# Optimization experiments

Measured on AMD Instinct MI355X. Metric: run time of the kernel, lower is better.

The kernel has to match this reference:

```python
import jax, jax.numpy as jnp
import numpy as np

N_SLOTS = 64
DECAY = 0.999
B, S, H, M = 4, 4096, 2048, 128


def _l2norm(t, eps=1e-12):
    return t / jnp.maximum(jnp.linalg.norm(t, axis=-1, keepdims=True), eps)


def setup_inputs() -> dict:
    key = jax.random.key(0)
    ks = jax.random.split(key, 6)
    return {
        "x": jax.random.normal(ks[0], (B, S, H), dtype=jnp.float32),
        "W_query": jax.random.normal(ks[1], (M, H), dtype=jnp.float32) * 0.02,
        "W_key": jax.random.normal(ks[2], (M, H), dtype=jnp.float32) * 0.02,
        "W_value": jax.random.normal(ks[3], (M, H), dtype=jnp.float32) * 0.02,
        "W_out": jax.random.normal(ks[4], (H, M), dtype=jnp.float32) * 0.02,
        "W_gate_w": jax.random.normal(ks[5], (1, H), dtype=jnp.float32) * 0.02,
        "W_gate_b": jnp.full((1,), -2.0, dtype=jnp.float32),
        "log_beta": jnp.full((1,), np.log(8.0), dtype=jnp.float32),
        "chunk_size": 64,
    }


def reference(x, W_query, W_key, W_value, W_out, W_gate_w, W_gate_b, log_beta, chunk_size):
    b, s, h = x.shape
    m = W_query.shape[0]
    dt = x.dtype

    q = x @ W_query.T                      # (b, s, m)
    k = _l2norm(x @ W_key.T)               # (b, s, m)
    v = _l2norm(x @ W_value.T)             # (b, s, m)
    gate = jax.nn.sigmoid(x @ W_gate_w.T + W_gate_b)  # (b, s, 1)
    beta = jnp.exp(log_beta).reshape(())

    nc = s // chunk_size
    decay_c = jnp.asarray(DECAY, dt) ** chunk_size

    def chunkify(t):
        # (b, s, d) -> (nc, b, chunk, d)
        return jnp.moveaxis(t.reshape(b, nc, chunk_size, -1), 1, 0)

    qc, kc, vc = chunkify(q), chunkify(k), chunkify(v)
    wc = chunkify(gate)[..., 0]            # (nc, b, chunk)

    K0 = jnp.zeros((N_SLOTS, m), dt)
    V0 = jnp.zeros((N_SLOTS, m), dt)
    s0 = jnp.zeros((N_SLOTS,), dt)
    ptr0 = jnp.asarray(0, jnp.int32)

    def step(carry, inp):
        K_mem, V_mem, mem_strength, ptr = carry
        qch, kch, vch, wch = inp           # (b,c,m) x3, (b,c)
        # --- read: softmax retrieval over active slots ---
        slot_mask = (mem_strength > 1e-8).astype(dt)           # (n_slots,)
        scores = jnp.einsum("bcm,nm->bcn", qch, K_mem) * beta
        scores = scores + (1.0 - slot_mask) * -1e9
        attn = jax.nn.softmax(scores, axis=-1)
        r = jnp.einsum("bcn,nm->bcm", attn, V_mem)
        r = jnp.where(mem_strength.sum() < 1e-8, jnp.zeros_like(r), r)
        # --- write: gated aggregation into one slot ---
        w_sum = jnp.maximum(wch.sum(), 1e-8)
        k_agg = _l2norm((kch * wch[..., None]).sum((0, 1)) / w_sum)
        v_agg = _l2norm((vch * wch[..., None]).sum((0, 1)) / w_sum)
        write_str = wch.mean()
        mem_strength = mem_strength * decay_c
        slot = ptr % N_SLOTS
        K_mem = K_mem.at[slot].set(k_agg)
        V_mem = V_mem.at[slot].set(v_agg)
        mem_strength = mem_strength.at[slot].set(write_str)
        return (K_mem, V_mem, mem_strength, ptr + 1), (r, write_str)

    _, (rs, wss) = jax.lax.scan(step, (K0, V0, s0, ptr0), (qc, kc, vc, wc))

    retrieved = jnp.moveaxis(rs, 0, 1).reshape(b, s, m)
    out = retrieved @ W_out.T              # (b, s, h)
    # clamp output norm to 10
    onorm = jnp.maximum(jnp.linalg.norm(out, axis=-1, keepdims=True), 1e-6)
    out = out * jnp.minimum(10.0 / onorm, 1.0)
    mean_ws = jnp.mean(wss)
    return out, mean_ws
```

## Files before the change

### kernel.cpp

```cpp
#include <hip/hip_runtime.h>
#include <math.h>
#include <stdint.h>

#define NTOK 16384
#define SEQ  4096
#define HD   2048
#define MD   128
#define NCH  64
#define CHK  64

typedef __attribute__((ext_vector_type(8))) _Float16 half8;
typedef __attribute__((ext_vector_type(4))) float floatx4;

__device__ __forceinline__ void gload_lds16(const void* g, void* l) {
    __builtin_amdgcn_global_load_lds(
        (const __attribute__((address_space(1))) unsigned int*)(uintptr_t)g,
        (__attribute__((address_space(3))) unsigned int*)(uintptr_t)l,
        16, 0, 0);
}

__global__ __launch_bounds__(256) void convert_w_kernel(
    const float* __restrict__ Wq, const float* __restrict__ Wk,
    const float* __restrict__ Wv, const float* __restrict__ Wo,
    _Float16* __restrict__ Wcath, _Float16* __restrict__ Woh)
{
    int i = blockIdx.x * 256 + threadIdx.x;
    if (i < 384 * HD) {
        int r = i >> 11;
        float val;
        if (r < 128)      val = Wq[i];
        else if (r < 256) val = Wk[i - 128 * HD];
        else              val = Wv[i - 256 * HD];
        Wcath[i] = (_Float16)val;
    } else {
        int j = i - 384 * HD;
        Woh[j] = (_Float16)Wo[j];
    }
}

__global__ __launch_bounds__(128) void gmat_kernel(
    const float* __restrict__ Wo, float* __restrict__ G)
{
    __shared__ float col[HD];
    int a = blockIdx.x;
    int b = threadIdx.x;
    for (int j = b; j < HD; j += 128) col[j] = Wo[(size_t)j * MD + a];
    __syncthreads();
    float s = 0.f;
    for (int j = 0; j < HD; ++j) s = fmaf(col[j], Wo[(size_t)j * MD + b], s);
    G[a * MD + b] = s;
}

__global__ __launch_bounds__(256, 1) void gemm_proj_mfma(
    const float* __restrict__ x, const _Float16* __restrict__ Wcath,
    const float* __restrict__ Wgw, const float* __restrict__ gb,
    float* __restrict__ q, float* __restrict__ k, float* __restrict__ v,
    float* __restrict__ wg)
{
    __shared__ _Float16 As[2][64 * 64];
    __shared__ _Float16 Bs[2][3][128 * 64];
    floatx4 acc[3][2][4];
    #pragma unroll
    for (int p = 0; p < 3; ++p)
        #pragma unroll
        for (int i = 0; i < 2; ++i)
            #pragma unroll
            for (int j = 0; j < 4; ++j) acc[p][i][j] = (floatx4){0.f, 0.f, 0.f, 0.f};

    const int tid  = threadIdx.x;
    const int wave = tid >> 6, lane = tid & 63;
    const int wm = wave & 1, wn = wave >> 1;
    const int row0 = blockIdx.x * 64;

    const int ar0 = tid >> 3;
    const int ac0 = (tid & 7) ^ (ar0 & 7);
    const float* xA0 = x + (size_t)(row0 + ar0) * HD + ac0 * 8;
    const float* xA1 = x + (size_t)(row0 + ar0 + 32) * HD + ac0 * 8;
    const float* wgp = Wgw + ac0 * 8;

    float gacc0 = 0.f, gacc1 = 0.f;
    float4 a00, a01, a10, a11, g0, g1;

#define STAGE_B(buf_, k0_) do {                                               \
        _Pragma("unroll")                                                     \
        for (int p = 0; p < 3; ++p) {                                         \
            _Pragma("unroll")                                                 \
            for (int rnd = 0; rnd < 4; ++rnd) {                               \
                int sg = rnd * 4 + wave;                                      \
                int br = sg * 8 + (lane >> 3);                                \
                int bc = (lane & 7) ^ (br & 7);                               \
                gload_lds16(Wcath + (size_t)(p * 128 + br) * HD + (k0_) + bc * 8, \
                            (char*)Bs[buf_][p] + sg * 1024);                  \
            }                                                                 \
        } } while (0)

#define LOAD_A(k0_) do {                                                      \
        a00 = *(const float4*)(xA0 + (k0_));                                  \
        a01 = *(const float4*)(xA0 + (k0_) + 4);                              \
        a10 = *(const float4*)(xA1 + (k0_));                                  \
        a11 = *(const float4*)(xA1 + (k0_) + 4);                              \
        g0 = *(const float4*)(wgp + (k0_));                                   \
        g1 = *(const float4*)(wgp + (k0_) + 4);                               \
    } while (0)

#define FINISH_A(buf_) do {                                                   \
        gacc0 += a00.x*g0.x + a00.y*g0.y + a00.z*g0.z + a00.w*g0.w            \
               + a01.x*g1.x + a01.y*g1.y + a01.z*g1.z + a01.w*g1.w;           \
        gacc1 += a10.x*g0.x + a10.y*g0.y + a10.z*g0.z + a10.w*g0.w            \
               + a11.x*g1.x + a11.y*g1.y + a11.z*g1.z + a11.w*g1.w;           \
        half8 h0, h1;                                                         \
        h0[0] = (_Float16)a00.x; h0[1] = (_Float16)a00.y;                     \
        h0[2] = (_Float16)a00.z; h0[3] = (_Float16)a00.w;                     \
        h0[4] = (_Float16)a01.x; h0[5] = (_Float16)a01.y;                     \
        h0[6] = (_Float16)a01.z; h0[7] = (_Float16)a01.w;                     \
        h1[0] = (_Float16)a10.x; h1[1] = (_Float16)a10.y;                     \
        h1[2] = (_Float16)a10.z; h1[3] = (_Float16)a10.w;                     \
        h1[4] = (_Float16)a11.x; h1[5] = (_Float16)a11.y;                     \
        h1[6] = (_Float16)a11.z; h1[7] = (_Float16)a11.w;                     \
        *(half8*)((char*)As[buf_] + tid * 16)        = h0;                    \
        *(half8*)((char*)As[buf_] + 4096 + tid * 16) = h1;                    \
    } while (0)

#define COMPUTE(buf_) do {                                                    \
        half8 af[2][2];                                                       \
        _Pragma("unroll")                                                     \
        for (int i = 0; i < 2; ++i) {                                         \
            int r  = wm * 32 + i * 16 + (lane & 15);                          \
            int rb = r * 128 + (lane >> 4) * 16;                              \
            int sw = (r & 7) << 4;                                            \
            af[i][0] = *(const half8*)((const char*)As[buf_] + ( rb       ^ sw)); \
            af[i][1] = *(const half8*)((const char*)As[buf_] + ((rb + 64) ^ sw)); \
        }                                                                     \
        _Pragma("unroll")                                                     \
        for (int p = 0; p < 3; ++p) {                                         \
            half8 bf[4][2];                                                   \
            _Pragma("unroll")                                                 \
            for (int j = 0; j < 4; ++j) {                                     \
                int r  = wn * 64 + j * 16 + (lane & 15);                      \
                int rb = r * 128 + (lane >> 4) * 16;                          \
                int sw = (r & 7) << 4;                                        \
                bf[j][0] = *(const half8*)((const char*)Bs[buf_][p] + ( rb       ^ sw)); \
                bf[j][1] = *(const half8*)((const char*)Bs[buf_][p] + ((rb + 64) ^ sw)); \
            }                                                                 \
            _Pragma("unroll")                                                 \
            for (int ks = 0; ks < 2; ++ks)                                    \
                _Pragma("unroll")                                             \
                for (int i = 0; i < 2; ++i)                                   \
                    _Pragma("unroll")                                         \
                    for (int j = 0; j < 4; ++j)                               \
                        acc[p][i][j] = __builtin_amdgcn_mfma_f32_16x16x32_f16(\
                            af[i][ks], bf[j][ks], acc[p][i][j], 0, 0, 0);     \
        }                                                                     \
    } while (0)

    STAGE_B(0, 0);
    LOAD_A(0);
    FINISH_A(0);
    __syncthreads();

    int cur = 0;
    for (int t = 0; t < HD / 64; ++t) {
        if (t < HD / 64 - 1) {
            STAGE_B(cur ^ 1, (t + 1) * 64);
            LOAD_A((t + 1) * 64);
        }
        COMPUTE(cur);
        if (t < HD / 64 - 1) FINISH_A(cur ^ 1);
        __syncthreads();
        cur ^= 1;
    }

    gacc0 += __shfl_xor(gacc0, 1);
    gacc0 += __shfl_xor(gacc0, 2);
    gacc0 += __shfl_xor(gacc0, 4);
    gacc1 += __shfl_xor(gacc1, 1);
    gacc1 += __shfl_xor(gacc1, 2);
    gacc1 += __shfl_xor(gacc1, 4);
    if ((tid & 7) == 0) {
        wg[row0 + ar0]      = 1.f / (1.f + expf(-(gacc0 + gb[0])));
        wg[row0 + ar0 + 32] = 1.f / (1.f + expf(-(gacc1 + gb[0])));
    }

    #pragma unroll
    for (int p = 0; p < 3; ++p) {
        float* dst = (p == 0) ? q : ((p == 1) ? k : v);
        #pragma unroll
        for (int i = 0; i < 2; ++i) {
            int m = row0 + wm * 32 + i * 16 + (lane >> 4) * 4;
            #pragma unroll
            for (int j = 0; j < 4; ++j) {
                int c = wn * 64 + j * 16 + (lane & 15);
                #pragma unroll
                for (int r = 0; r < 4; ++r)
                    dst[(size_t)(m + r) * MD + c] = acc[p][i][j][r];
            }
        }
    }
#undef STAGE_B
#undef LOAD_A
#undef FINISH_A
#undef COMPUTE
}

__global__ __launch_bounds__(256) void normsig_kernel(
    float* __restrict__ k, float* __restrict__ v)
{
    int wave = threadIdx.x >> 6, lane = threadIdx.x & 63;
    int row = blockIdx.x * 4 + wave;
    size_t base = (size_t)row * MD + lane * 2;
    float2 k2 = *reinterpret_cast<float2*>(&k[base]);
    float2 v2 = *reinterpret_cast<float2*>(&v[base]);
    float ks = k2.x * k2.x + k2.y * k2.y;
    float vs = v2.x * v2.x + v2.y * v2.y;
    #pragma unroll
    for (int off = 32; off > 0; off >>= 1) {
        ks += __shfl_xor(ks, off);
        vs += __shfl_xor(vs, off);
    }
    float ki = 1.f / fmaxf(sqrtf(ks), 1e-12f);
    float vi = 1.f / fmaxf(sqrtf(vs), 1e-12f);
    k2.x *= ki; k2.y *= ki; v2.x *= vi; v2.y *= vi;
    *reinterpret_cast<float2*>(&k[base]) = k2;
    *reinterpret_cast<float2*>(&v[base]) = v2;
}

__global__ __launch_bounds__(256) void agg_part_kernel(
    const float* __restrict__ kn, const float* __restrict__ vn,
    const float* __restrict__ w,
    float* __restrict__ kpart, float* __restrict__ vpart,
    float* __restrict__ wpart)
{
    int t = blockIdx.x >> 2, b = blockIdx.x & 3;
    int tid = threadIdx.x;
    int d = tid & 127, h = tid >> 7;
    int base_row = b * SEQ + t * CHK;

    float ka = 0.f, va = 0.f;
    for (int c = h * 32; c < h * 32 + 32; ++c) {
        int row = base_row + c;
        float wv = w[row];
        ka = fmaf(wv, kn[(size_t)row * MD + d], ka);
        va = fmaf(wv, vn[(size_t)row * MD + d], va);
    }
    __shared__ float sk[128], sv[128];
    if (h == 1) { sk[d] = ka; sv[d] = va; }
    __syncthreads();
    if (h == 0) {
        kpart[(size_t)blockIdx.x * 128 + d] = ka + sk[d];
        vpart[(size_t)blockIdx.x * 128 + d] = va + sv[d];
    }
    if (tid < 64) {
        float wv = w[base_row + tid];
        #pragma unroll
        for (int off = 32; off > 0; off >>= 1) wv += __shfl_xor(wv, off);
        if (tid == 0) wpart[blockIdx.x] = wv;
    }
}

__global__ __launch_bounds__(128) void agg_combine_kernel(
    const float* __restrict__ kpart, const float* __restrict__ vpart,
    const float* __restrict__ wpart,
    float* __restrict__ kaT, float* __restrict__ vagg, float* __restrict__ wstr)
{
    int t = blockIdx.x;
    int d = threadIdx.x;
    int wave = d >> 6, lane = d & 63;
    float ku = 0.f, vu = 0.f;
    #pragma unroll
    for (int b = 0; b < 4; ++b) {
        ku += kpart[(size_t)(t * 4 + b) * 128 + d];
        vu += vpart[(size_t)(t * 4 + b) * 128 + d];
    }
    float wsum = wpart[t * 4] + wpart[t * 4 + 1] + wpart[t * 4 + 2] + wpart[t * 4 + 3];
    float winv = 1.f / fmaxf(wsum, 1e-8f);
    ku *= winv; vu *= winv;

    __shared__ float red[4];
    float ks = ku * ku, vs = vu * vu;
    #pragma unroll
    for (int off = 32; off > 0; off >>= 1) {
        ks += __shfl_xor(ks, off);
        vs += __shfl_xor(vs, off);
    }
    if (lane == 0) { red[wave] = ks; red[2 + wave] = vs; }
    __syncthreads();
    float kinv = 1.f / fmaxf(sqrtf(red[0] + red[1]), 1e-12f);
    float vinv = 1.f / fmaxf(sqrtf(red[2] + red[3]), 1e-12f);
    kaT[d * NCH + t] = ku * kinv;
    vagg[t * MD + d] = vu * vinv;
    if (d == 0) wstr[t] = wsum * (1.f / 256.f);
}

__global__ __launch_bounds__(64) void meanws_kernel(
    const float* __restrict__ wstr, float* __restrict__ outp)
{
    int lane = threadIdx.x;
    float v = wstr[lane];
    #pragma unroll
    for (int off = 32; off > 0; off >>= 1) v += __shfl_xor(v, off);
    if (lane == 0) outp[0] = v * (1.f / 64.f);
}

__global__ __launch_bounds__(512, 1) void attn_kernel(
    const float* __restrict__ q, const float* __restrict__ kaT,
    const float* __restrict__ vagg, const float* __restrict__ G,
    const float* __restrict__ logbeta, _Float16* __restrict__ rsh16)
{
    __shared__ float kaT_s[MD * NCH];
    __shared__ float vagg_s[NCH * MD];
    __shared__ float G_s[MD * MD];
    __shared__ float qs[8][MD];
    __shared__ float attn_sh[8][64];
    __shared__ float rsh_sh[8][MD];

    const int tid  = threadIdx.x;
    const int wave = tid >> 6, lane = tid & 63;
    const int row0 = blockIdx.x * 64;
    const int t = (row0 & (SEQ - 1)) >> 6;
    const float beta = expf(logbeta[0]);

    {
        const float4* s0 = (const float4*)kaT;
        const float4* s1 = (const float4*)vagg;
        const float4* s2 = (const float4*)G;
        float4* d0 = (float4*)kaT_s;
        float4* d1 = (float4*)vagg_s;
        float4* d2 = (float4*)G_s;
        #pragma unroll
        for (int i = 0; i < 4; ++i) {
            d0[tid + i * 512] = s0[tid + i * 512];
            d1[tid + i * 512] = s1[tid + i * 512];
        }
        #pragma unroll
        for (int i = 0; i < 8; ++i)
            d2[tid + i * 512] = s2[tid + i * 512];
    }
    __syncthreads();

    for (int rr = 0; rr < 8; ++rr) {
        const int row = row0 + wave * 8 + rr;
        float q0 = q[(size_t)row * MD + lane];
        float q1 = q[(size_t)row * MD + 64 + lane];
        qs[wave][lane]      = q0;
        qs[wave][lane + 64] = q1;

        float sc = -INFINITY;
        if (lane < t) {
            sc = 0.f;
            for (int d = 0; d < 128; ++d)
                sc = fmaf(qs[wave][d], kaT_s[d * NCH + lane], sc);
            sc *= beta;
        }
        float mx = sc;
        #pragma unroll
        for (int off = 32; off > 0; off >>= 1) mx = fmaxf(mx, __shfl_xor(mx, off));
        float e = (lane < t) ? expf(sc - mx) : 0.f;
        float ssum = e;
        #pragma unroll
        for (int off = 32; off > 0; off >>= 1) ssum += __shfl_xor(ssum, off);
        float attn = (t > 0) ? (e / ssum) : 0.f;
        attn_sh[wave][lane] = attn;

        float r0 = 0.f, r1 = 0.f;
        for (int n = 0; n < t; ++n) {
            float a = attn_sh[wave][n];
            r0 = fmaf(a, vagg_s[n * MD + lane], r0);
            r1 = fmaf(a, vagg_s[n * MD + 64 + lane], r1);
        }
        rsh_sh[wave][lane]      = r0;
        rsh_sh[wave][lane + 64] = r1;

        float t0 = 0.f, t1 = 0.f;
        for (int b = 0; b < 128; ++b) {
            float rb = rsh_sh[wave][b];
            t0 = fmaf(G_s[b * MD + lane], rb, t0);
            t1 = fmaf(G_s[b * MD + 64 + lane], rb, t1);
        }
        float quad = r0 * t0 + r1 * t1;
        #pragma unroll
        for (int off = 32; off > 0; off >>= 1) quad += __shfl_xor(quad, off);
        float nrm = fmaxf(sqrtf(fmaxf(quad, 0.f)), 1e-6f);
        float scl = fminf(10.f / nrm, 1.f);
        rsh16[(size_t)row * MD + lane]      = (_Float16)(r0 * scl);
        rsh16[(size_t)row * MD + 64 + lane] = (_Float16)(r1 * scl);
    }
}

__global__ __launch_bounds__(256) void gemm_out_mfma(
    const _Float16* __restrict__ rsh16, const _Float16* __restrict__ Woh,
    float* __restrict__ C)
{
    __shared__ _Float16 As[128 * 128];
    __shared__ _Float16 Bs[128 * 128];
    floatx4 acc[4][4];
    #pragma unroll
    for (int i = 0; i < 4; ++i)
        #pragma unroll
        for (int j = 0; j < 4; ++j) acc[i][j] = (floatx4){0.f, 0.f, 0.f, 0.f};

    const int tid  = threadIdx.x;
    const int wave = tid >> 6, lane = tid & 63;
    const int wm = wave & 1, wn = wave >> 1;
    const int row0 = blockIdx.x * 128;
    const int col0 = blockIdx.y * 128;

    const int sr = lane >> 4;
    const int sp = lane & 15;
    #pragma unroll
    for (int rnd = 0; rnd < 8; ++rnd) {
        int seg = wave * 8 + rnd;
        int r = seg * 4 + sr;
        int c = sp ^ (r & 15);
        gload_lds16(rsh16 + (size_t)(row0 + r) * MD + c * 8,
                    (char*)As + seg * 1024);
        gload_lds16(Woh + (size_t)(col0 + r) * MD + c * 8,
                    (char*)Bs + seg * 1024);
    }
    __syncthreads();

    #pragma unroll
    for (int kf = 0; kf < 4; ++kf) {
        half8 af[4], bf[4];
        #pragma unroll
        for (int i = 0; i < 4; ++i) {
            int r = wm * 64 + i * 16 + (lane & 15);
            int g = kf * 4 + (lane >> 4);
            af[i] = *(const half8*)((const char*)As + r * 256 + ((g ^ (r & 15)) * 16));
        }
        #pragma unroll
        for (int j = 0; j < 4; ++j) {
            int r = wn * 64 + j * 16 + (lane & 15);
            int g = kf * 4 + (lane >> 4);
            bf[j] = *(const half8*)((const char*)Bs + r * 256 + ((g ^ (r & 15)) * 16));
        }
        #pragma unroll
        for (int i = 0; i < 4; ++i)
            #pragma unroll
            for (int j = 0; j < 4; ++j)
                acc[i][j] = __builtin_amdgcn_mfma_f32_16x16x32_f16(
                    af[i], bf[j], acc[i][j], 0, 0, 0);
    }

    #pragma unroll
    for (int i = 0; i < 4; ++i) {
        int m = row0 + wm * 64 + i * 16 + (lane >> 4) * 4;
        #pragma unroll
        for (int j = 0; j < 4; ++j) {
            int c = col0 + wn * 64 + j * 16 + (lane & 15);
            #pragma unroll
            for (int r = 0; r < 4; ++r)
                C[(size_t)(m + r) * HD + c] = acc[i][j][r];
        }
    }
}

extern "C" void kernel_launch(void* const* d_in, const int* in_sizes, int n_in,
                              void* d_out, int out_size, void* d_ws, size_t ws_size,
                              hipStream_t stream)
{
    const float* x   = (const float*)d_in[0];
    const float* Wq  = (const float*)d_in[1];
    const float* Wk  = (const float*)d_in[2];
    const float* Wv  = (const float*)d_in[3];
    const float* Wo  = (const float*)d_in[4];
    const float* Wgw = (const float*)d_in[5];
    const float* Wgb = (const float*)d_in[6];
    const float* lb  = (const float*)d_in[7];
    float* out = (float*)d_out;

    float* q    = (float*)d_ws;
    float* kn   = q + (size_t)NTOK * MD;
    float* vn   = kn + (size_t)NTOK * MD;
    float* wg   = vn + (size_t)NTOK * MD;
    float* kaT  = wg + NTOK;
    float* vagg = kaT + MD * NCH;
    float* wstr = vagg + NCH * MD;
    float* G    = wstr + 64;
    float* kpart = G + MD * MD;
    float* vpart = kpart + 256 * 128;
    float* wpart = vpart + 256 * 128;
    _Float16* Wcath = (_Float16*)(wpart + 256);
    _Float16* Woh   = Wcath + 384 * HD;
    _Float16* rsh16 = Woh + HD * MD;

    convert_w_kernel<<<dim3(4096), dim3(256), 0, stream>>>(Wq, Wk, Wv, Wo, Wcath, Woh);
    gmat_kernel<<<dim3(128), dim3(128), 0, stream>>>(Wo, G);
    gemm_proj_mfma<<<dim3(NTOK / 64), dim3(256), 0, stream>>>(
        x, Wcath, Wgw, Wgb, q, kn, vn, wg);
    normsig_kernel<<<dim3(NTOK / 4), dim3(256), 0, stream>>>(kn, vn);
    agg_part_kernel<<<dim3(256), dim3(256), 0, stream>>>(kn, vn, wg, kpart, vpart, wpart);
    agg_combine_kernel<<<dim3(NCH), dim3(128), 0, stream>>>(kpart, vpart, wpart, kaT, vagg, wstr);
    meanws_kernel<<<dim3(1), dim3(64), 0, stream>>>(wstr, out + (size_t)NTOK * HD);
    attn_kernel<<<dim3(NTOK / 64), dim3(512), 0, stream>>>(q, kaT, vagg, G, lb, rsh16);
    gemm_out_mfma<<<dim3(NTOK / 128, HD / 128), dim3(256), 0, stream>>>(rsh16, Woh, out);
}
```

Measured before the change: 393.5 us.

## Fuse k/v L2 normalization and chunk aggregation into projection GEMM epilogue

The projection GEMM epilogue now stages k and v tiles in reused shared memory, L2-normalizes each row there, and computes the gated per-chunk partial sums directly. The separate normsig and agg_part kernels are removed, along with the global writes and reads of k, v and the gate. This saves two launches and about 16 MB of global traffic. In exchange the epilogue gets longer and has extra barriers, and it relies on each 64-row block lining up with exactly one chunk of one batch.

```diff
diff --git a/kernel.cpp b/kernel.cpp
--- a/kernel.cpp
+++ b/kernel.cpp
@@ -54,8 +54,9 @@
 __global__ __launch_bounds__(256, 1) void gemm_proj_mfma(
     const float* __restrict__ x, const _Float16* __restrict__ Wcath,
     const float* __restrict__ Wgw, const float* __restrict__ gb,
-    float* __restrict__ q, float* __restrict__ k, float* __restrict__ v,
-    float* __restrict__ wg)
+    float* __restrict__ q,
+    float* __restrict__ kpart, float* __restrict__ vpart,
+    float* __restrict__ wpart)
 {
     __shared__ _Float16 As[2][64 * 64];
     __shared__ _Float16 Bs[2][3][128 * 64];
@@ -170,6 +171,23 @@
         cur ^= 1;
     }
 
+    float* k_s   = (float*)&Bs[0][0][0];
+    float* v_s   = k_s + 64 * 128;
+    float* ws_s  = (float*)&As[0][0];
+    float* red_s = ws_s + 64;
+
+    #pragma unroll
+    for (int i = 0; i < 2; ++i) {
+        int m = row0 + wm * 32 + i * 16 + (lane >> 4) * 4;
+        #pragma unroll
+        for (int j = 0; j < 4; ++j) {
+            int c = wn * 64 + j * 16 + (lane & 15);
+            #pragma unroll
+            for (int r = 0; r < 4; ++r)
+                q[(size_t)(m + r) * MD + c] = acc[0][i][j][r];
+        }
+    }
+
     gacc0 += __shfl_xor(gacc0, 1);
     gacc0 += __shfl_xor(gacc0, 2);
     gacc0 += __shfl_xor(gacc0, 4);
@@ -177,84 +195,74 @@
     gacc1 += __shfl_xor(gacc1, 2);
     gacc1 += __shfl_xor(gacc1, 4);
     if ((tid & 7) == 0) {
-        wg[row0 + ar0]      = 1.f / (1.f + expf(-(gacc0 + gb[0])));
-        wg[row0 + ar0 + 32] = 1.f / (1.f + expf(-(gacc1 + gb[0])));
-    }
-
-    #pragma unroll
-    for (int p = 0; p < 3; ++p) {
-        float* dst = (p == 0) ? q : ((p == 1) ? k : v);
-        #pragma unroll
-        for (int i = 0; i < 2; ++i) {
-            int m = row0 + wm * 32 + i * 16 + (lane >> 4) * 4;
+        ws_s[ar0]      = 1.f / (1.f + expf(-(gacc0 + gb[0])));
+        ws_s[ar0 + 32] = 1.f / (1.f + expf(-(gacc1 + gb[0])));
+    }
+
+    #pragma unroll
+    for (int i = 0; i < 2; ++i) {
+        int m = wm * 32 + i * 16 + (lane >> 4) * 4;
+        #pragma unroll
+        for (int j = 0; j < 4; ++j) {
+            int c = wn * 64 + j * 16 + (lane & 15);
             #pragma unroll
-            for (int j = 0; j < 4; ++j) {
-                int c = wn * 64 + j * 16 + (lane & 15);
-                #pragma unroll
-                for (int r = 0; r < 4; ++r)
-                    dst[(size_t)(m + r) * MD + c] = acc[p][i][j][r];
+            for (int r = 0; r < 4; ++r) {
+                k_s[(m + r) * 128 + c] = acc[1][i][j][r];
+                v_s[(m + r) * 128 + c] = acc[2][i][j][r];
             }
+        }
+    }
+    __syncthreads();
+
+    #pragma unroll
+    for (int rr = 0; rr < 16; ++rr) {
+        int row = wave * 16 + rr;
+        float kx = k_s[row * 128 + 2 * lane];
+        float ky = k_s[row * 128 + 2 * lane + 1];
+        float vx = v_s[row * 128 + 2 * lane];
+        float vy = v_s[row * 128 + 2 * lane + 1];
+        float ks = kx * kx + ky * ky;
+        float vs = vx * vx + vy * vy;
+        #pragma unroll
+        for (int off = 32; off > 0; off >>= 1) {
+            ks += __shfl_xor(ks, off);
+            vs += __shfl_xor(vs, off);
+        }
+        float ki = 1.f / fmaxf(sqrtf(ks), 1e-12f);
+        float vi = 1.f / fmaxf(sqrtf(vs), 1e-12f);
+        k_s[row * 128 + 2 * lane]     = kx * ki;
+        k_s[row * 128 + 2 * lane + 1] = ky * ki;
+        v_s[row * 128 + 2 * lane]     = vx * vi;
+        v_s[row * 128 + 2 * lane + 1] = vy * vi;
+    }
+    __syncthreads();
+
+    {
+        const int d = tid & 127, h = tid >> 7;
+        float ka = 0.f, va = 0.f;
+        for (int c = h * 32; c < h * 32 + 32; ++c) {
+            float wv = ws_s[c];
+            ka = fmaf(wv, k_s[c * 128 + d], ka);
+            va = fmaf(wv, v_s[c * 128 + d], va);
+        }
+        if (h == 1) { red_s[d] = ka; red_s[128 + d] = va; }
+        __syncthreads();
+        const int bidx = ((row0 & (SEQ - 1)) >> 6) * 4 + (row0 >> 12);
+        if (h == 0) {
+            kpart[(size_t)bidx * 128 + d] = ka + red_s[d];
+            vpart[(size_t)bidx * 128 + d] = va + red_s[128 + d];
+        }
+        if (tid < 64) {
+            float wv = ws_s[tid];
+            #pragma unroll
+            for (int off = 32; off > 0; off >>= 1) wv += __shfl_xor(wv, off);
+            if (tid == 0) wpart[bidx] = wv;
         }
     }
 #undef STAGE_B
 #undef LOAD_A
 #undef FINISH_A
 #undef COMPUTE
-}
-
-__global__ __launch_bounds__(256) void normsig_kernel(
-    float* __restrict__ k, float* __restrict__ v)
-{
-    int wave = threadIdx.x >> 6, lane = threadIdx.x & 63;
-    int row = blockIdx.x * 4 + wave;
-    size_t base = (size_t)row * MD + lane * 2;
-    float2 k2 = *reinterpret_cast<float2*>(&k[base]);
-    float2 v2 = *reinterpret_cast<float2*>(&v[base]);
-    float ks = k2.x * k2.x + k2.y * k2.y;
-    float vs = v2.x * v2.x + v2.y * v2.y;
-    #pragma unroll
-    for (int off = 32; off > 0; off >>= 1) {
-        ks += __shfl_xor(ks, off);
-        vs += __shfl_xor(vs, off);
-    }
-    float ki = 1.f / fmaxf(sqrtf(ks), 1e-12f);
-    float vi = 1.f / fmaxf(sqrtf(vs), 1e-12f);
-    k2.x *= ki; k2.y *= ki; v2.x *= vi; v2.y *= vi;
-    *reinterpret_cast<float2*>(&k[base]) = k2;
-    *reinterpret_cast<float2*>(&v[base]) = v2;
-}
-
-__global__ __launch_bounds__(256) void agg_part_kernel(
-    const float* __restrict__ kn, const float* __restrict__ vn,
-    const float* __restrict__ w,
-    float* __restrict__ kpart, float* __restrict__ vpart,
-    float* __restrict__ wpart)
-{
-    int t = blockIdx.x >> 2, b = blockIdx.x & 3;
-    int tid = threadIdx.x;
-    int d = tid & 127, h = tid >> 7;
-    int base_row = b * SEQ + t * CHK;
-
-    float ka = 0.f, va = 0.f;
-    for (int c = h * 32; c < h * 32 + 32; ++c) {
-        int row = base_row + c;
-        float wv = w[row];
-        ka = fmaf(wv, kn[(size_t)row * MD + d], ka);
-        va = fmaf(wv, vn[(size_t)row * MD + d], va);
-    }
-    __shared__ float sk[128], sv[128];
-    if (h == 1) { sk[d] = ka; sv[d] = va; }
-    __syncthreads();
-    if (h == 0) {
-        kpart[(size_t)blockIdx.x * 128 + d] = ka + sk[d];
-        vpart[(size_t)blockIdx.x * 128 + d] = va + sv[d];
-    }
-    if (tid < 64) {
-        float wv = w[base_row + tid];
-        #pragma unroll
-        for (int off = 32; off > 0; off >>= 1) wv += __shfl_xor(wv, off);
-        if (tid == 0) wpart[blockIdx.x] = wv;
-    }
 }
 
 __global__ __launch_bounds__(128) void agg_combine_kernel(
@@ -486,9 +494,7 @@
     convert_w_kernel<<<dim3(4096), dim3(256), 0, stream>>>(Wq, Wk, Wv, Wo, Wcath, Woh);
     gmat_kernel<<<dim3(128), dim3(128), 0, stream>>>(Wo, G);
     gemm_proj_mfma<<<dim3(NTOK / 64), dim3(256), 0, stream>>>(
-        x, Wcath, Wgw, Wgb, q, kn, vn, wg);
-    normsig_kernel<<<dim3(NTOK / 4), dim3(256), 0, stream>>>(kn, vn);
-    agg_part_kernel<<<dim3(256), dim3(256), 0, stream>>>(kn, vn, wg, kpart, vpart, wpart);
+        x, Wcath, Wgw, Wgb, q, kpart, vpart, wpart);
     agg_combine_kernel<<<dim3(NCH), dim3(128), 0, stream>>>(kpart, vpart, wpart, kaT, vagg, wstr);
     meanws_kernel<<<dim3(1), dim3(64), 0, stream>>>(wstr, out + (size_t)NTOK * HD);
     attn_kernel<<<dim3(NTOK / 64), dim3(512), 0, stream>>>(q, kaT, vagg, G, lb, rsh16);
```

After: 407.7 us. 3.6% more time.
